# Performance work log

Hardware: AMD Instinct MI355X
Metric: run time of the kernel (lower is better)

Reference implementation:

```python
import jax, jax.numpy as jnp
import numpy as np

N = 100000
E = 800000
D_IN = 64
D_OUT = 64
SCALES = (4, 8)


def setup_inputs() -> dict:
    key = jax.random.key(0)
    ks = jax.random.split(key, 8)
    x = jax.random.normal(ks[0], (N, D_IN), dtype=jnp.float32)
    edge_index = jax.random.randint(ks[1], (2, E), 0, N, dtype=jnp.int64)
    s = 1.0 / np.sqrt(D_IN)
    W1 = jax.random.uniform(ks[2], (D_OUT, D_IN), minval=-s, maxval=s, dtype=jnp.float32)
    b1 = jax.random.uniform(ks[3], (D_OUT,), minval=-s, maxval=s, dtype=jnp.float32)
    W2 = jax.random.uniform(ks[4], (D_OUT, D_IN), minval=-s, maxval=s, dtype=jnp.float32)
    b2 = jax.random.uniform(ks[5], (D_OUT,), minval=-s, maxval=s, dtype=jnp.float32)
    sg = 1.0 / np.sqrt(D_OUT * len(SCALES))
    Wg = jax.random.uniform(ks[6], (D_OUT, D_OUT * len(SCALES)), minval=-sg, maxval=sg, dtype=jnp.float32)
    bg = jax.random.uniform(ks[7], (D_OUT,), minval=-sg, maxval=sg, dtype=jnp.float32)
    return {"x": x, "edge_index": edge_index, "W1": W1, "b1": b1,
            "W2": W2, "b2": b2, "Wg": Wg, "bg": bg}


def _gconv(x, src, tgt, W, b):
    # scatter-add neighbor features: agg[src] += x[tgt]
    agg = jax.ops.segment_sum(x[tgt], src, num_segments=N)  # [N, D_IN]
    counts = jax.ops.segment_sum(jnp.ones((src.shape[0], 1), x.dtype), src,
                                 num_segments=N) + 1e-6     # [N, 1]
    agg = agg / counts
    return agg @ W.T + b                                    # [N, D_OUT]


def reference(x, edge_index, W1, b1, W2, b2, Wg, bg):
    k_max = E // N  # = 8
    outs = []
    for scale, (W, b) in zip(SCALES, ((W1, b1), (W2, b2))):
        scale = min(scale, k_max)
        src = edge_index[0, :N * scale]
        tgt = edge_index[1, :N * scale]
        outs.append(_gconv(x, src, tgt, W, b))
    multi = jnp.concatenate(outs, axis=-1)                   # [N, 2*D_OUT]
    gate = jax.nn.sigmoid(multi @ Wg.T + bg)                 # [N, D_OUT]
    fused = gate * outs[0] + (1.0 - gate) * outs[1]
    return fused
```

## Files before the change

kernel.cpp:

```cpp
#include <hip/hip_runtime.h>
#include <hip/hip_bf16.h>

#define N_NODES 100000
#define E_TOTAL 800000
#define E1      400000
#define D       64
#define CAP     32

#define NPB        256
#define NB         ((N_NODES + NPB - 1) / NPB)
#define BSTRIDE    (NPB * CAP)
#define EPB        4096
#define NBKT_BLKS  ((E_TOTAL + EPB - 1) / EPB)
#define PER        40
#define SPAN       (NBKT_BLKS * PER)
#define PREP_TPB   512
#define EPT        (EPB / PREP_TPB)

typedef short s16x8 __attribute__((ext_vector_type(8)));
typedef float f32x4 __attribute__((ext_vector_type(4)));
typedef unsigned u32x4 __attribute__((ext_vector_type(4)));

#define WS_CNT     0
#define WS_ENTRIES (N_NODES)
#define WS_W1B     (WS_ENTRIES + N_NODES * CAP)
#define WS_W2B     (WS_W1B + 2048)
#define WS_WGB     (WS_W2B + 2048)
#define WS_BIAS    (WS_WGB + 4096)
#define WS_REC390  (WS_BIAS + 192)
#define WS_XB      (WS_REC390 + SPAN)
#define WS_NEED_BYTES ((size_t)(WS_XB + (size_t)N_NODES * D / 2) * 4)

#define XCONV_BLOCKS ((N_NODES * D / 16 + PREP_TPB - 1) / PREP_TPB)
#define WCONV_BLOCKS 5

__device__ __forceinline__ float ldv(const void* p, size_t idx, int fp32)
{
    return fp32 ? ((const float*)p)[idx]
                : __bfloat162float(((const __hip_bfloat16*)p)[idx]);
}

__device__ __forceinline__ void detect2(const int* ei, const unsigned short* xu,
                                        int* s2, int& e64, int& fp32)
{
    if (threadIdx.x == 0) { s2[0] = 0; s2[1] = 0; }
    __syncthreads();
    if (threadIdx.x < 16 && ei[2 * threadIdx.x + 1] != 0) atomicOr(&s2[0], 1);
    { unsigned u = xu[threadIdx.x]; if (((u >> 7) & 0xFF) >= 0x90) atomicOr(&s2[1], 1); }
    __syncthreads();
    e64 = (s2[0] == 0); fp32 = s2[1];
}

__global__ __launch_bounds__(512) void prep_kernel(
    const void* __restrict__ xv, const int* __restrict__ ei,
    const void* __restrict__ W1v, const void* __restrict__ b1v,
    const void* __restrict__ W2v, const void* __restrict__ b2v,
    const void* __restrict__ Wgv, const void* __restrict__ bgv,
    unsigned* __restrict__ ws, int use_xb)
{
    __shared__ int s2[2];
    __shared__ unsigned hist[512];
    __shared__ __align__(16) unsigned cells[NB * PER];

    int e64, fp32;
    detect2(ei, (const unsigned short*)xv, s2, e64, fp32);

    const int tid = threadIdx.x;

    if (blockIdx.x < NBKT_BLKS) {
        hist[tid] = 0;
        {
            const u32x4 z = {0u, 0u, 0u, 0u};
            for (int j = tid; j < NB * PER / 4; j += PREP_TPB) ((u32x4*)cells)[j] = z;
        }
        __syncthreads();

        const int e0 = blockIdx.x * EPB;
        int srcv[EPT], tgtv[EPT];
        if (e64) {
#pragma unroll
            for (int i = 0; i < EPT; ++i) {
                const int e  = e0 + i * PREP_TPB + tid;
                const int ec = min(e, E_TOTAL - 1);
                srcv[i] = (int)((const uint2*)ei)[ec].x;
                tgtv[i] = (int)((const uint2*)ei)[E_TOTAL + ec].x;
                if (e >= E_TOTAL) srcv[i] = -1;
            }
        } else {
#pragma unroll
            for (int i = 0; i < EPT; ++i) {
                const int e  = e0 + i * PREP_TPB + tid;
                const int ec = min(e, E_TOTAL - 1);
                srcv[i] = ei[ec];
                tgtv[i] = ei[E_TOTAL + ec];
                if (e >= E_TOTAL) srcv[i] = -1;
            }
        }

#pragma unroll
        for (int i = 0; i < EPT; ++i) {
            const int e = e0 + i * PREP_TPB + tid;
            if (srcv[i] >= 0) {
                const unsigned b = (unsigned)srcv[i] >> 8;
                const unsigned r = atomicAdd(&hist[b], 1u);
                if (r < PER)
                    cells[b * PER + r] = (unsigned)tgtv[i]
                                       | ((e < E1) ? 0x20000u : 0u)
                                       | (((unsigned)srcv[i] & 0xFFu) << 18)
                                       | 0x80000000u;
            }
        }
        __syncthreads();

        unsigned* dstbase = ws + WS_ENTRIES + (size_t)blockIdx.x * PER;
        unsigned* rec390  = ws + WS_REC390 + (size_t)blockIdx.x * PER;
        for (int j = tid; j < NB * PER; j += PREP_TPB) {
            const int b = j / PER;
            const int r = j - b * PER;
            if (b == NB - 1) rec390[r] = cells[j];
            else             dstbase[(size_t)b * BSTRIDE + r] = cells[j];
        }
        return;
    }

    const int bx = (int)blockIdx.x - NBKT_BLKS;
    if (bx < XCONV_BLOCKS) {
        if (use_xb && fp32) {
            const int gid = bx * PREP_TPB + tid;
            if (gid < N_NODES * D / 16) {
                __hip_bfloat16* Xb = (__hip_bfloat16*)(ws + WS_XB);
                const f32x4* src4 = (const f32x4*)xv + (size_t)gid * 4;
#pragma unroll
                for (int h = 0; h < 2; ++h) {
                    const f32x4 v0 = src4[2 * h];
                    const f32x4 v1 = src4[2 * h + 1];
                    s16x8 o;
#pragma unroll
                    for (int j = 0; j < 4; ++j) {
                        o[j]     = (short)__bfloat16_as_ushort(__float2bfloat16(v0[j]));
                        o[4 + j] = (short)__bfloat16_as_ushort(__float2bfloat16(v1[j]));
                    }
                    *(s16x8*)(Xb + (size_t)gid * 16 + h * 8) = o;
                }
            }
        }
        return;
    }

    const int gid = (bx - XCONV_BLOCKS) * PREP_TPB + tid;
    __hip_bfloat16* W1b = (__hip_bfloat16*)(ws + WS_W1B);
    __hip_bfloat16* W2b = (__hip_bfloat16*)(ws + WS_W2B);
    __hip_bfloat16* Wgb = (__hip_bfloat16*)(ws + WS_WGB);
    float* bias = (float*)(ws + WS_BIAS);

    if (gid < 2048) {
#pragma unroll
        for (int k = 0; k < 8; ++k) {
            const int i = gid * 8 + k;
            if (i < 4096)       W1b[i]        = __float2bfloat16(ldv(W1v, i, fp32));
            else if (i < 8192)  W2b[i - 4096] = __float2bfloat16(ldv(W2v, i - 4096, fp32));
            else                Wgb[i - 8192] = __float2bfloat16(ldv(Wgv, i - 8192, fp32));
        }
    } else if (gid < 2072) {
        const int j = gid - 2048;
#pragma unroll
        for (int k = 0; k < 8; ++k) {
            const int i = j * 8 + k;
            if (i < 64)       bias[i] = ldv(b1v, i, fp32);
            else if (i < 128) bias[i] = ldv(b2v, i - 64, fp32);
            else              bias[i] = ldv(bgv, i - 128, fp32);
        }
    }
}

__global__ __launch_bounds__(256) void csr_kernel(unsigned* __restrict__ ws)
{
    __shared__ __align__(16) unsigned rec_s[SPAN];
    __shared__ __align__(16) unsigned ent[NPB * CAP];
    __shared__ unsigned n1c[NPB], ctc[NPB], a1[NPB], a2[NPB];

    const int b  = blockIdx.x;
    const int n0 = b * NPB;
    const int nn = min(NPB, N_NODES - n0);
    const unsigned* span = (b == NB - 1) ? (ws + WS_REC390)
                                         : (ws + WS_ENTRIES + (size_t)b * BSTRIDE);

    if (threadIdx.x < NPB) { n1c[threadIdx.x] = 0; ctc[threadIdx.x] = 0; }
    {
        const u32x4 z = {0u, 0u, 0u, 0u};
        for (int j = threadIdx.x; j < NPB * CAP / 4; j += 256) ((u32x4*)ent)[j] = z;
        for (int j = threadIdx.x; j < SPAN / 4; j += 256)
            ((u32x4*)rec_s)[j] = ((const u32x4*)span)[j];
    }
    __syncthreads();

    for (int r = threadIdx.x; r < SPAN; r += 256) {
        const unsigned rec = rec_s[r];
        if (rec & 0x80000000u) {
            const unsigned sl = (rec >> 18) & 0xFFu;
            atomicAdd(&ctc[sl], 1u);
            if (rec & 0x20000u) atomicAdd(&n1c[sl], 1u);
        }
    }
    __syncthreads();
    if (threadIdx.x < NPB) {
        a1[threadIdx.x] = 0u;
        a2[threadIdx.x] = min(n1c[threadIdx.x], (unsigned)CAP);
    }
    __syncthreads();
    for (int r = threadIdx.x; r < SPAN; r += 256) {
        const unsigned rec = rec_s[r];
        if (rec & 0x80000000u) {
            const unsigned sl = (rec >> 18) & 0xFFu;
            unsigned p;
            if (rec & 0x20000u) p = atomicAdd(&a1[sl], 1u);
            else                p = atomicAdd(&a2[sl], 1u);
            if (p < CAP) ent[sl * CAP + p] = rec & 0x1FFFFu;
        }
    }
    __syncthreads();

    const int tot4 = (nn * CAP) / 4;
    u32x4* dst = (u32x4*)(ws + WS_ENTRIES + (size_t)n0 * CAP);
    const u32x4* srcp = (const u32x4*)ent;
    for (int j = threadIdx.x; j < tot4; j += 256) dst[j] = srcp[j];

    if (threadIdx.x < nn) {
        const unsigned ct = min(ctc[threadIdx.x], 0xFFFFu);
        const unsigned p1 = min(n1c[threadIdx.x], (unsigned)CAP);
        ws[WS_CNT + n0 + threadIdx.x] = ct | (p1 << 16);
    }
}

__global__ __launch_bounds__(256) void fused_kernel(
    const unsigned* __restrict__ ws, const void* __restrict__ xv,
    void* __restrict__ outv, int use_xb)
{
    __shared__ __align__(16) __hip_bfloat16 sS[16][136];
    __shared__ __align__(16) __hip_bfloat16 sO[16][136];
    __shared__ int s2d[1];

    if (threadIdx.x == 0) s2d[0] = 0;
    __syncthreads();
    { unsigned u = ((const unsigned short*)xv)[threadIdx.x];
      if (((u >> 7) & 0xFF) >= 0x90) atomicOr(&s2d[0], 1); }
    __syncthreads();
    const int fp32 = s2d[0];

    const int w    = threadIdx.x >> 6;
    const int lane = threadIdx.x & 63;
    const int base = blockIdx.x * 16;

    unsigned entv[4], cw[4];
#pragma unroll
    for (int i = 0; i < 4; ++i) {
        const int n = base + w * 4 + i;
        cw[i]   = ws[WS_CNT + n];
        entv[i] = ws[WS_ENTRIES + (size_t)n * CAP + (lane & 31)];
    }
    int degc[4], p1c[4]; unsigned degt[4];
#pragma unroll
    for (int i = 0; i < 4; ++i) {
        degt[i] = cw[i] & 0xFFFFu;
        p1c[i]  = (int)(cw[i] >> 16);
        degc[i] = (int)min(degt[i], (unsigned)CAP);
    }

    const int half = lane >> 5;
    const int cc   = lane & 31;

    float s1x[4], s1y[4], s2x[4], s2y[4];
#pragma unroll
    for (int i = 0; i < 4; ++i) { s1x[i] = s1y[i] = s2x[i] = s2y[i] = 0.f; }

    int rmax = 0;
#pragma unroll
    for (int i = 0; i < 4; ++i) rmax = max(rmax, (degc[i] + 1) >> 1);
    rmax = (rmax + 1) & ~1;

    const int direct_f32 = (fp32 && !use_xb);
    if (!direct_f32) {
        const char* xb = fp32 ? (const char*)(ws + WS_XB) : (const char*)xv;
        const unsigned ccb = (unsigned)cc << 2;
#pragma unroll 2
        for (int r = 0; r < rmax; ++r) {
#pragma unroll
            for (int i = 0; i < 4; ++i) {
                const int j = 2 * r + half;
                const unsigned en = (unsigned)__shfl((int)entv[i], j);
                unsigned u = *(const unsigned*)(xb + (size_t)((en << 7) + ccb));
                u = (j < degc[i]) ? u : 0u;
                const float fx = __uint_as_float(u << 16);
                const float fy = __uint_as_float(u & 0xFFFF0000u);
                const float fl = (j < p1c[i]) ? 1.f : 0.f;
                s2x[i] += fx; s2y[i] += fy;
                s1x[i] = fmaf(fl, fx, s1x[i]); s1y[i] = fmaf(fl, fy, s1y[i]);
            }
        }
    } else {
        const char* xb = (const char*)xv;
        const unsigned ccb = (unsigned)cc << 3;
#pragma unroll 2
        for (int r = 0; r < rmax; ++r) {
#pragma unroll
            for (int i = 0; i < 4; ++i) {
                const int j = 2 * r + half;
                const unsigned en = (unsigned)__shfl((int)entv[i], j);
                const uint2 u = *(const uint2*)(xb + (size_t)((en << 8) + ccb));
                const bool val = j < degc[i];
                const float fx = val ? __uint_as_float(u.x) : 0.f;
                const float fy = val ? __uint_as_float(u.y) : 0.f;
                const float fl = (j < p1c[i]) ? 1.f : 0.f;
                s2x[i] += fx; s2y[i] += fy;
                s1x[i] = fmaf(fl, fx, s1x[i]); s1y[i] = fmaf(fl, fy, s1y[i]);
            }
        }
    }

#pragma unroll
    for (int i = 0; i < 4; ++i) {
        const int nl = w * 4 + i;
        float a = s1x[i], b = s1y[i], c = s2x[i], d = s2y[i];
        a += __shfl_xor(a, 32); b += __shfl_xor(b, 32);
        c += __shfl_xor(c, 32); d += __shfl_xor(d, 32);
        const float inv1 = 1.0f / ((float)p1c[i] + 1e-6f);
        const float inv2 = 1.0f / ((float)degt[i] + 1e-6f);
        if (lane < 32) {
            const __hip_bfloat162 p1 = __float22bfloat162_rn({a * inv1, b * inv1});
            const __hip_bfloat162 p2 = __float22bfloat162_rn({c * inv2, d * inv2});
            *(__hip_bfloat162*)&sS[nl][2 * cc]      = p1;
            *(__hip_bfloat162*)&sS[nl][64 + 2 * cc] = p2;
        }
    }
    __syncthreads();

    const int m = lane & 15;
    const int q = lane >> 4;
    const int nd = w * 16 + m;

    const s16x8* W1b = (const s16x8*)(ws + WS_W1B);
    const s16x8* W2b = (const s16x8*)(ws + WS_W2B);
    const s16x8* Wgb = (const s16x8*)(ws + WS_WGB);
    const float* bias = (const float*)(ws + WS_BIAS);

    const s16x8 a1c0 = *(const s16x8*)&sS[m][q * 8];
    const s16x8 a1c1 = *(const s16x8*)&sS[m][32 + q * 8];
    const s16x8 a2c0 = *(const s16x8*)&sS[m][64 + q * 8];
    const s16x8 a2c1 = *(const s16x8*)&sS[m][96 + q * 8];

    f32x4 z = {0.f, 0.f, 0.f, 0.f};
    z = __builtin_amdgcn_mfma_f32_16x16x32_bf16(a1c0, W1b[nd * 8 + q],     z, 0, 0, 0);
    z = __builtin_amdgcn_mfma_f32_16x16x32_bf16(a1c1, W1b[nd * 8 + 4 + q], z, 0, 0, 0);
    f32x4 y = {0.f, 0.f, 0.f, 0.f};
    y = __builtin_amdgcn_mfma_f32_16x16x32_bf16(a2c0, W2b[nd * 8 + q],     y, 0, 0, 0);
    y = __builtin_amdgcn_mfma_f32_16x16x32_bf16(a2c1, W2b[nd * 8 + 4 + q], y, 0, 0, 0);
    const float bb1 = bias[nd], bb2 = bias[64 + nd];
#pragma unroll
    for (int r = 0; r < 4; ++r) { z[r] += bb1; y[r] += bb2; }

#pragma unroll
    for (int r = 0; r < 4; ++r) {
        sO[q * 4 + r][nd]      = __float2bfloat16(z[r]);
        sO[q * 4 + r][64 + nd] = __float2bfloat16(y[r]);
    }
    __syncthreads();

    s16x8 ga[4];
#pragma unroll
    for (int c = 0; c < 4; ++c)
        ga[c] = *(const s16x8*)&sO[m][c * 32 + q * 8];

    f32x4 g4 = {0.f, 0.f, 0.f, 0.f};
#pragma unroll
    for (int c = 0; c < 4; ++c)
        g4 = __builtin_amdgcn_mfma_f32_16x16x32_bf16(ga[c], Wgb[nd * 16 + c * 4 + q], g4, 0, 0, 0);
    const float bbg = bias[128 + nd];

#pragma unroll
    for (int r = 0; r < 4; ++r) {
        const float g = 1.0f / (1.0f + __expf(-(g4[r] + bbg)));
        const float v = g * z[r] + (1.0f - g) * y[r];
        const size_t node = (size_t)(base + q * 4 + r);
        if (fp32) ((float*)outv)[node * 64 + nd] = v;
        else      ((__hip_bfloat16*)outv)[node * 64 + nd] = __float2bfloat16(v);
    }
}

extern "C" void kernel_launch(void* const* d_in, const int* in_sizes, int n_in,
                              void* d_out, int out_size, void* d_ws, size_t ws_size,
                              hipStream_t stream)
{
    const void* x  = d_in[0];
    const int*  ei = (const int*)d_in[1];
    unsigned* ws = (unsigned*)d_ws;

    const int use_xb = (ws_size >= WS_NEED_BYTES) ? 1 : 0;

    prep_kernel<<<NBKT_BLKS + XCONV_BLOCKS + WCONV_BLOCKS, PREP_TPB, 0, stream>>>(
        x, ei, d_in[2], d_in[3], d_in[4], d_in[5], d_in[6], d_in[7], ws, use_xb);
    csr_kernel<<<NB, 256, 0, stream>>>(ws);
    fused_kernel<<<N_NODES / 16, 256, 0, stream>>>(ws, x, d_out, use_xb);
}
```

Measured before the change: 153.3 us.

## Move x/weight bf16 conversion from prep kernel into CSR kernel launch

The fp32-to-bf16 conversion of x and the weight/bias conversion move out of the edge-bucketing prep kernel and into extra blocks of the CSR kernel. The CSR build now reads span records straight from global memory in 16-byte vectors instead of staging them in shared memory. The aim is to shorten the prep kernel's critical path, cut the CSR kernel's LDS footprint so more blocks fit per CU, and overlap the conversion with the CSR build. In exchange the span is read from global memory twice, and the CSR kernel's grid is larger, using 256-thread grid-stride conversion blocks.

```diff
diff --git a/kernel.cpp b/kernel.cpp
--- a/kernel.cpp
+++ b/kernel.cpp
@@ -31,8 +31,9 @@
 #define WS_XB      (WS_REC390 + SPAN)
 #define WS_NEED_BYTES ((size_t)(WS_XB + (size_t)N_NODES * D / 2) * 4)
 
-#define XCONV_BLOCKS ((N_NODES * D / 16 + PREP_TPB - 1) / PREP_TPB)
-#define WCONV_BLOCKS 5
+#define CSR_XCONV  782
+#define CSR_WCONV  9
+#define CSR_TPB    256
 
 __device__ __forceinline__ float ldv(const void* p, size_t idx, int fp32)
 {
@@ -40,114 +41,174 @@
                 : __bfloat162float(((const __hip_bfloat16*)p)[idx]);
 }
 
-__device__ __forceinline__ void detect2(const int* ei, const unsigned short* xu,
-                                        int* s2, int& e64, int& fp32)
+__global__ __launch_bounds__(512) void prep_kernel(
+    const int* __restrict__ ei, unsigned* __restrict__ ws)
 {
-    if (threadIdx.x == 0) { s2[0] = 0; s2[1] = 0; }
-    __syncthreads();
-    if (threadIdx.x < 16 && ei[2 * threadIdx.x + 1] != 0) atomicOr(&s2[0], 1);
-    { unsigned u = xu[threadIdx.x]; if (((u >> 7) & 0xFF) >= 0x90) atomicOr(&s2[1], 1); }
-    __syncthreads();
-    e64 = (s2[0] == 0); fp32 = s2[1];
+    __shared__ int s2[1];
+    __shared__ unsigned hist[512];
+    __shared__ __align__(16) unsigned cells[NB * PER];
+
+    const int tid = threadIdx.x;
+
+    if (tid == 0) s2[0] = 0;
+    __syncthreads();
+    if (tid < 16 && ei[2 * tid + 1] != 0) atomicOr(&s2[0], 1);
+    hist[tid] = 0;
+    {
+        const u32x4 z = {0u, 0u, 0u, 0u};
+        for (int j = tid; j < NB * PER / 4; j += PREP_TPB) ((u32x4*)cells)[j] = z;
+    }
+    __syncthreads();
+    const int e64 = (s2[0] == 0);
+
+    const int e0 = blockIdx.x * EPB;
+    int srcv[EPT], tgtv[EPT];
+    if (e64) {
+#pragma unroll
+        for (int i = 0; i < EPT; ++i) {
+            const int e  = e0 + i * PREP_TPB + tid;
+            const int ec = min(e, E_TOTAL - 1);
+            srcv[i] = (int)((const uint2*)ei)[ec].x;
+            tgtv[i] = (int)((const uint2*)ei)[E_TOTAL + ec].x;
+            if (e >= E_TOTAL) srcv[i] = -1;
+        }
+    } else {
+#pragma unroll
+        for (int i = 0; i < EPT; ++i) {
+            const int e  = e0 + i * PREP_TPB + tid;
+            const int ec = min(e, E_TOTAL - 1);
+            srcv[i] = ei[ec];
+            tgtv[i] = ei[E_TOTAL + ec];
+            if (e >= E_TOTAL) srcv[i] = -1;
+        }
+    }
+
+#pragma unroll
+    for (int i = 0; i < EPT; ++i) {
+        const int e = e0 + i * PREP_TPB + tid;
+        if (srcv[i] >= 0) {
+            const unsigned b = (unsigned)srcv[i] >> 8;
+            const unsigned r = atomicAdd(&hist[b], 1u);
+            if (r < PER)
+                cells[b * PER + r] = (unsigned)tgtv[i]
+                                   | ((e < E1) ? 0x20000u : 0u)
+                                   | (((unsigned)srcv[i] & 0xFFu) << 18)
+                                   | 0x80000000u;
+        }
+    }
+    __syncthreads();
+
+    unsigned* dstbase = ws + WS_ENTRIES + (size_t)blockIdx.x * PER;
+    unsigned* rec390  = ws + WS_REC390 + (size_t)blockIdx.x * PER;
+    for (int j = tid; j < NB * PER; j += PREP_TPB) {
+        const int b = j / PER;
+        const int r = j - b * PER;
+        if (b == NB - 1) rec390[r] = cells[j];
+        else             dstbase[(size_t)b * BSTRIDE + r] = cells[j];
+    }
 }
 
-__global__ __launch_bounds__(512) void prep_kernel(
-    const void* __restrict__ xv, const int* __restrict__ ei,
+__global__ __launch_bounds__(256) void csr_kernel(
+    const void* __restrict__ xv,
     const void* __restrict__ W1v, const void* __restrict__ b1v,
     const void* __restrict__ W2v, const void* __restrict__ b2v,
     const void* __restrict__ Wgv, const void* __restrict__ bgv,
     unsigned* __restrict__ ws, int use_xb)
 {
-    __shared__ int s2[2];
-    __shared__ unsigned hist[512];
-    __shared__ __align__(16) unsigned cells[NB * PER];
-
-    int e64, fp32;
-    detect2(ei, (const unsigned short*)xv, s2, e64, fp32);
+    __shared__ __align__(16) unsigned ent[NPB * CAP];
+    __shared__ unsigned n1c[NPB], ctc[NPB], a1[NPB], a2[NPB];
+    __shared__ int s2[1];
 
     const int tid = threadIdx.x;
 
-    if (blockIdx.x < NBKT_BLKS) {
-        hist[tid] = 0;
+    if (blockIdx.x < NB) {
+        const int b  = blockIdx.x;
+        const int n0 = b * NPB;
+        const int nn = min(NPB, N_NODES - n0);
+        const u32x4* span4 = (const u32x4*)((b == NB - 1)
+                              ? (ws + WS_REC390)
+                              : (ws + WS_ENTRIES + (size_t)b * BSTRIDE));
+
+        n1c[tid] = 0; ctc[tid] = 0;
         {
             const u32x4 z = {0u, 0u, 0u, 0u};
-            for (int j = tid; j < NB * PER / 4; j += PREP_TPB) ((u32x4*)cells)[j] = z;
+            for (int j = tid; j < NPB * CAP / 4; j += CSR_TPB) ((u32x4*)ent)[j] = z;
         }
         __syncthreads();
 
-        const int e0 = blockIdx.x * EPB;
-        int srcv[EPT], tgtv[EPT];
-        if (e64) {
-#pragma unroll
-            for (int i = 0; i < EPT; ++i) {
-                const int e  = e0 + i * PREP_TPB + tid;
-                const int ec = min(e, E_TOTAL - 1);
-                srcv[i] = (int)((const uint2*)ei)[ec].x;
-                tgtv[i] = (int)((const uint2*)ei)[E_TOTAL + ec].x;
-                if (e >= E_TOTAL) srcv[i] = -1;
-            }
-        } else {
-#pragma unroll
-            for (int i = 0; i < EPT; ++i) {
-                const int e  = e0 + i * PREP_TPB + tid;
-                const int ec = min(e, E_TOTAL - 1);
-                srcv[i] = ei[ec];
-                tgtv[i] = ei[E_TOTAL + ec];
-                if (e >= E_TOTAL) srcv[i] = -1;
-            }
-        }
-
-#pragma unroll
-        for (int i = 0; i < EPT; ++i) {
-            const int e = e0 + i * PREP_TPB + tid;
-            if (srcv[i] >= 0) {
-                const unsigned b = (unsigned)srcv[i] >> 8;
-                const unsigned r = atomicAdd(&hist[b], 1u);
-                if (r < PER)
-                    cells[b * PER + r] = (unsigned)tgtv[i]
-                                       | ((e < E1) ? 0x20000u : 0u)
-                                       | (((unsigned)srcv[i] & 0xFFu) << 18)
-                                       | 0x80000000u;
-            }
-        }
-        __syncthreads();
-
-        unsigned* dstbase = ws + WS_ENTRIES + (size_t)blockIdx.x * PER;
-        unsigned* rec390  = ws + WS_REC390 + (size_t)blockIdx.x * PER;
-        for (int j = tid; j < NB * PER; j += PREP_TPB) {
-            const int b = j / PER;
-            const int r = j - b * PER;
-            if (b == NB - 1) rec390[r] = cells[j];
-            else             dstbase[(size_t)b * BSTRIDE + r] = cells[j];
-        }
-        return;
-    }
-
-    const int bx = (int)blockIdx.x - NBKT_BLKS;
-    if (bx < XCONV_BLOCKS) {
-        if (use_xb && fp32) {
-            const int gid = bx * PREP_TPB + tid;
-            if (gid < N_NODES * D / 16) {
-                __hip_bfloat16* Xb = (__hip_bfloat16*)(ws + WS_XB);
-                const f32x4* src4 = (const f32x4*)xv + (size_t)gid * 4;
-#pragma unroll
-                for (int h = 0; h < 2; ++h) {
-                    const f32x4 v0 = src4[2 * h];
-                    const f32x4 v1 = src4[2 * h + 1];
-                    s16x8 o;
-#pragma unroll
-                    for (int j = 0; j < 4; ++j) {
-                        o[j]     = (short)__bfloat16_as_ushort(__float2bfloat16(v0[j]));
-                        o[4 + j] = (short)__bfloat16_as_ushort(__float2bfloat16(v1[j]));
-                    }
-                    *(s16x8*)(Xb + (size_t)gid * 16 + h * 8) = o;
+        for (int r4 = tid; r4 < SPAN / 4; r4 += CSR_TPB) {
+            const u32x4 q = span4[r4];
+#pragma unroll
+            for (int k = 0; k < 4; ++k) {
+                const unsigned rec = q[k];
+                if (rec & 0x80000000u) {
+                    const unsigned sl = (rec >> 18) & 0xFFu;
+                    atomicAdd(&ctc[sl], 1u);
+                    if (rec & 0x20000u) atomicAdd(&n1c[sl], 1u);
                 }
             }
         }
+        __syncthreads();
+        a1[tid] = 0u;
+        a2[tid] = min(n1c[tid], (unsigned)CAP);
+        __syncthreads();
+        for (int r4 = tid; r4 < SPAN / 4; r4 += CSR_TPB) {
+            const u32x4 q = span4[r4];
+#pragma unroll
+            for (int k = 0; k < 4; ++k) {
+                const unsigned rec = q[k];
+                if (rec & 0x80000000u) {
+                    const unsigned sl = (rec >> 18) & 0xFFu;
+                    unsigned p;
+                    if (rec & 0x20000u) p = atomicAdd(&a1[sl], 1u);
+                    else                p = atomicAdd(&a2[sl], 1u);
+                    if (p < CAP) ent[sl * CAP + p] = rec & 0x1FFFFu;
+                }
+            }
+        }
+        __syncthreads();
+
+        const int tot4 = (nn * CAP) / 4;
+        u32x4* dst = (u32x4*)(ws + WS_ENTRIES + (size_t)n0 * CAP);
+        const u32x4* srcp = (const u32x4*)ent;
+        for (int j = tid; j < tot4; j += CSR_TPB) dst[j] = srcp[j];
+
+        if (tid < nn) {
+            const unsigned ct = min(ctc[tid], 0xFFFFu);
+            const unsigned p1 = min(n1c[tid], (unsigned)CAP);
+            ws[WS_CNT + n0 + tid] = ct | (p1 << 16);
+        }
         return;
     }
 
-    const int gid = (bx - XCONV_BLOCKS) * PREP_TPB + tid;
+    if (tid == 0) s2[0] = 0;
+    __syncthreads();
+    { unsigned u = ((const unsigned short*)xv)[tid];
+      if (((u >> 7) & 0xFF) >= 0x90) atomicOr(&s2[0], 1); }
+    __syncthreads();
+    const int fp32 = s2[0];
+
+    const int bx = (int)blockIdx.x - NB;
+    if (bx < CSR_XCONV) {
+        if (use_xb && fp32) {
+            __hip_bfloat16* Xb = (__hip_bfloat16*)(ws + WS_XB);
+            const int nthr = CSR_XCONV * CSR_TPB;
+            for (int c = bx * CSR_TPB + tid; c < N_NODES * D / 8; c += nthr) {
+                const f32x4 v0 = ((const f32x4*)xv)[2 * c];
+                const f32x4 v1 = ((const f32x4*)xv)[2 * c + 1];
+                s16x8 o;
+#pragma unroll
+                for (int j = 0; j < 4; ++j) {
+                    o[j]     = (short)__bfloat16_as_ushort(__float2bfloat16(v0[j]));
+                    o[4 + j] = (short)__bfloat16_as_ushort(__float2bfloat16(v1[j]));
+                }
+                *(s16x8*)(Xb + (size_t)c * 8) = o;
+            }
+        }
+        return;
+    }
+
+    const int gid = (bx - CSR_XCONV) * CSR_TPB + tid;
     __hip_bfloat16* W1b = (__hip_bfloat16*)(ws + WS_W1B);
     __hip_bfloat16* W2b = (__hip_bfloat16*)(ws + WS_W2B);
     __hip_bfloat16* Wgb = (__hip_bfloat16*)(ws + WS_WGB);
@@ -170,65 +231,6 @@
             else if (i < 128) bias[i] = ldv(b2v, i - 64, fp32);
             else              bias[i] = ldv(bgv, i - 128, fp32);
         }
-    }
-}
-
-__global__ __launch_bounds__(256) void csr_kernel(unsigned* __restrict__ ws)
-{
-    __shared__ __align__(16) unsigned rec_s[SPAN];
-    __shared__ __align__(16) unsigned ent[NPB * CAP];
-    __shared__ unsigned n1c[NPB], ctc[NPB], a1[NPB], a2[NPB];
-
-    const int b  = blockIdx.x;
-    const int n0 = b * NPB;
-    const int nn = min(NPB, N_NODES - n0);
-    const unsigned* span = (b == NB - 1) ? (ws + WS_REC390)
-                                         : (ws + WS_ENTRIES + (size_t)b * BSTRIDE);
-
-    if (threadIdx.x < NPB) { n1c[threadIdx.x] = 0; ctc[threadIdx.x] = 0; }
-    {
-        const u32x4 z = {0u, 0u, 0u, 0u};
-        for (int j = threadIdx.x; j < NPB * CAP / 4; j += 256) ((u32x4*)ent)[j] = z;
-        for (int j = threadIdx.x; j < SPAN / 4; j += 256)
-            ((u32x4*)rec_s)[j] = ((const u32x4*)span)[j];
-    }
-    __syncthreads();
-
-    for (int r = threadIdx.x; r < SPAN; r += 256) {
-        const unsigned rec = rec_s[r];
-        if (rec & 0x80000000u) {
-            const unsigned sl = (rec >> 18) & 0xFFu;
-            atomicAdd(&ctc[sl], 1u);
-            if (rec & 0x20000u) atomicAdd(&n1c[sl], 1u);
-        }
-    }
-    __syncthreads();
-    if (threadIdx.x < NPB) {
-        a1[threadIdx.x] = 0u;
-        a2[threadIdx.x] = min(n1c[threadIdx.x], (unsigned)CAP);
-    }
-    __syncthreads();
-    for (int r = threadIdx.x; r < SPAN; r += 256) {
-        const unsigned rec = rec_s[r];
-        if (rec & 0x80000000u) {
-            const unsigned sl = (rec >> 18) & 0xFFu;
-            unsigned p;
-            if (rec & 0x20000u) p = atomicAdd(&a1[sl], 1u);
-            else                p = atomicAdd(&a2[sl], 1u);
-            if (p < CAP) ent[sl * CAP + p] = rec & 0x1FFFFu;
-        }
-    }
-    __syncthreads();
-
-    const int tot4 = (nn * CAP) / 4;
-    u32x4* dst = (u32x4*)(ws + WS_ENTRIES + (size_t)n0 * CAP);
-    const u32x4* srcp = (const u32x4*)ent;
-    for (int j = threadIdx.x; j < tot4; j += 256) dst[j] = srcp[j];
-
-    if (threadIdx.x < nn) {
-        const unsigned ct = min(ctc[threadIdx.x], 0xFFFFu);
-        const unsigned p1 = min(n1c[threadIdx.x], (unsigned)CAP);
-        ws[WS_CNT + n0 + threadIdx.x] = ct | (p1 << 16);
     }
 }
 
@@ -396,8 +398,8 @@
 
     const int use_xb = (ws_size >= WS_NEED_BYTES) ? 1 : 0;
 
-    prep_kernel<<<NBKT_BLKS + XCONV_BLOCKS + WCONV_BLOCKS, PREP_TPB, 0, stream>>>(
-        x, ei, d_in[2], d_in[3], d_in[4], d_in[5], d_in[6], d_in[7], ws, use_xb);
-    csr_kernel<<<NB, 256, 0, stream>>>(ws);
+    prep_kernel<<<NBKT_BLKS, PREP_TPB, 0, stream>>>(ei, ws);
+    csr_kernel<<<NB + CSR_XCONV + CSR_WCONV, CSR_TPB, 0, stream>>>(
+        x, d_in[2], d_in[3], d_in[4], d_in[5], d_in[6], d_in[7], ws, use_xb);
     fused_kernel<<<N_NODES / 16, 256, 0, stream>>>(ws, x, d_out, use_xb);
 }
```

Result: faster. 148.7 us (-3.0%).
